# Optimization experiments

Hardware: AMD Instinct MI355X
Metric: run time of the kernel (lower is better)

## Reference

```python
import jax, jax.numpy as jnp
import numpy as np

V = 16000      # vocab_size
D = 256        # embedding_dim
H = 512        # hidden_size (bi-LSTM concat)
HD = H // 2    # per-direction hidden
LAB = 32       # labelset_size (30 tags + START/STOP)
T = 512        # seq length
B = 128        # batch
START = 30
STOP = 31
NEG = -10000.0


def setup_inputs() -> dict:
    key = jax.random.key(0)
    ks = jax.random.split(key, 16)
    sc = 0.05
    emb = jax.random.normal(ks[0], (V, D), jnp.float32) * 0.1
    W_ih_f = jax.random.normal(ks[1], (4 * HD, D), jnp.float32) * sc
    W_hh_f = jax.random.normal(ks[2], (4 * HD, HD), jnp.float32) * sc
    b_f = jax.random.normal(ks[3], (4 * HD,), jnp.float32) * sc  # b_ih + b_hh combined
    W_ih_b = jax.random.normal(ks[4], (4 * HD, D), jnp.float32) * sc
    W_hh_b = jax.random.normal(ks[5], (4 * HD, HD), jnp.float32) * sc
    b_b = jax.random.normal(ks[6], (4 * HD,), jnp.float32) * sc
    Wo = jax.random.normal(ks[7], (LAB, H), jnp.float32) * sc
    bo = jnp.zeros((LAB,), jnp.float32)
    transitions = jax.random.normal(ks[8], (LAB, LAB), jnp.float32)
    transitions = transitions.at[STOP, :].set(NEG).at[:, START].set(NEG)
    h0 = jax.random.normal(ks[9], (2, B, HD), jnp.float32)  # init_hidden() uses randn
    c0 = jax.random.normal(ks[10], (2, B, HD), jnp.float32)
    sentences = jax.random.randint(ks[11], (T, B), 0, V, dtype=jnp.int32)
    labels = jax.random.randint(ks[12], (T, B), 0, 30, dtype=jnp.int32)
    masks = jnp.ones((T, B), dtype=bool)
    return {"emb": emb, "W_ih_f": W_ih_f, "W_hh_f": W_hh_f, "b_f": b_f,
            "W_ih_b": W_ih_b, "W_hh_b": W_hh_b, "b_b": b_b,
            "Wo": Wo, "bo": bo, "transitions": transitions,
            "h0": h0, "c0": c0,
            "sentences": sentences, "labels": labels, "masks": masks}


def _lstm_dir(xproj, h0, c0, W_hh):
    # xproj: [T, B, 4*HD] precomputed input projection (+bias)
    def step(carry, xg):
        h, c = carry
        g = xg + h @ W_hh.T
        i, f, gg, o = jnp.split(g, 4, axis=-1)  # torch gate order i,f,g,o
        i = jax.nn.sigmoid(i); f = jax.nn.sigmoid(f)
        gg = jnp.tanh(gg); o = jax.nn.sigmoid(o)
        c = f * c + i * gg
        h = o * jnp.tanh(c)
        return (h, c), h
    _, hs = jax.lax.scan(step, (h0, c0), xproj)
    return hs  # [T, B, HD]


def reference(emb, W_ih_f, W_hh_f, b_f, W_ih_b, W_hh_b, b_b, Wo, bo,
              transitions, h0, c0, sentences, labels, masks):
    # ---- encoder (dropout omitted: eval-mode determinism) ----
    x = emb[sentences]                                   # [T, B, D]
    xf = jnp.einsum('tbd,gd->tbg', x, W_ih_f) + b_f
    hf = _lstm_dir(xf, h0[0], c0[0], W_hh_f)             # [T, B, HD]
    xb = jnp.einsum('tbd,gd->tbg', x, W_ih_b) + b_b
    hb = _lstm_dir(xb[::-1], h0[1], c0[1], W_hh_b)[::-1]
    out = jnp.concatenate([hf, hb], axis=-1)             # [T, B, H]
    feats = jnp.einsum('tbh,lh->tbl', out, Wo) + bo      # [T, B, LAB]

    # ---- CRF forward algorithm (log partition) ----
    dp0 = jnp.full((B, LAB), NEG, jnp.float32).at[:, START].set(0.0)
    def fstep(dp, inp):
        sc, m = inp  # sc: [B, LAB], m: [B]
        new = jax.scipy.special.logsumexp(
            dp[:, :, None] + transitions[None, :, :] + sc[:, None, :], axis=1)
        return jnp.where(m[:, None], new, dp), None
    dpZ, _ = jax.lax.scan(fstep, dp0, (feats, masks))
    Z = jax.scipy.special.logsumexp(dpZ, axis=1)         # [B]

    # ---- gold path score ----
    lab_ext = jnp.concatenate(
        [jnp.full((1, B), START, labels.dtype), labels], axis=0)  # [T+1, B]
    bidx = jnp.arange(B)
    def gstep(dp, inp):
        sc, m, lp, ln = inp
        tmp = dp + transitions[lp, ln] + sc[bidx, ln]
        return jnp.where(m, tmp, dp), None
    gold, _ = jax.lax.scan(gstep, jnp.zeros((B,), jnp.float32),
                           (feats, masks, lab_ext[:-1], lab_ext[1:]))

    return (Z - gold).sum() / B
```

## Files before the change

kernel.cpp:

```cpp
#include <hip/hip_runtime.h>
#include <stdint.h>

typedef __attribute__((ext_vector_type(8))) short short8;
typedef __attribute__((ext_vector_type(4))) float floatx4;
typedef unsigned int u32;
typedef unsigned short u16;
typedef unsigned long long u64;

#define NROW 65536
#define RING 32

#define OFF_TAGS  64
#define OFF_READY 256
#define OFF_WIH   8192
#define OFF_WHH8  1056768
#define OFF_WO    2105344
#define OFF_RING  2138112
#define OFF_OUT   19177472
#define OFF_FE    86286336
#define WS_NEED   94674944

__device__ __forceinline__ u16 f2bf(float f){
  union { float f; u32 u; } v; v.f = f;
  u32 u = v.u;
  return (u16)((u + 0x7FFFu + ((u >> 16) & 1u)) >> 16);
}
__device__ __forceinline__ float bf2f(u16 h){
  union { u32 u; float f; } v; v.u = ((u32)h) << 16; return v.f;
}
__device__ __forceinline__ u32 pack2(float a, float b){
  return (u32)f2bf(a) | ((u32)f2bf(b) << 16);
}
__device__ __forceinline__ u32 pk_fp8x4(float a, float b, float c, float d){
  u32 lo = __builtin_amdgcn_cvt_pk_fp8_f32(a, b, 0, false);
  return (u32)__builtin_amdgcn_cvt_pk_fp8_f32(c, d, lo, true);
}
__device__ __forceinline__ float sigm(float x){
  return __builtin_amdgcn_rcpf(1.f + __expf(-x));
}
__device__ __forceinline__ float tanh_(float x){
  return 1.f - 2.f * __builtin_amdgcn_rcpf(1.f + __expf(2.f * x));
}
__device__ __forceinline__ floatx4 MF(short8 a, short8 b, floatx4 c){
  return __builtin_amdgcn_mfma_f32_16x16x32_bf16(a, b, c, 0, 0, 0);
}
__device__ __forceinline__ floatx4 MF8(long a, long b, floatx4 c){
  return __builtin_amdgcn_mfma_f32_16x16x32_fp8_fp8(a, b, c, 0, 0, 0);
}
__device__ __forceinline__ void ldsload16(const void* g, void* l){
  __builtin_amdgcn_global_load_lds(
      (const __attribute__((address_space(1))) u32*)g,
      (__attribute__((address_space(3))) u32*)l, 16, 0, 17);
}

__global__ void kdiag(float* out, float v){
  if (threadIdx.x == 0 && blockIdx.x == 0) out[0] = v;
}

__global__ void k0(const float* wf, const float* wb, const float* hf, const float* hb,
                   const float* wo, u16* wih, u16* wob, unsigned char* whh8){
  int e = blockIdx.x * 256 + threadIdx.x;
  if (e < 524288){ wih[e] = f2bf(e < 262144 ? wf[e] : wb[e - 262144]); return; }
  if (e < 540672){ wob[e - 524288] = f2bf(wo[e - 524288]); return; }
  if (e < 1064960){
    int t = e - 540672;
    float w = (t < 262144) ? hf[t] : hb[t - 262144];
    whh8[t] = (unsigned char)(__builtin_amdgcn_cvt_pk_fp8_f32(w, w, 0, false) & 0xFF);
  }
}

__launch_bounds__(512, 1)
__global__ void klstm(const float* emb, const int* sent, const u16* wih,
                      const float* bf_, const float* bb_,
                      const unsigned char* whh8, const float* h0, const float* c0,
                      char* ring, u16* outb, u32* ct, u32* ready){
  __shared__ __align__(16) char SH[98304];
  const int tid = threadIdx.x, n = tid >> 6, l15 = tid & 15, q = (tid >> 4) & 3;
  const int bid = blockIdx.x;

  if (bid >= 32){
    const int p = bid - 32, dir = p & 1;
    const float* bias = dir ? bb_ : bf_;
    int pbud = 1 << 20;
    for (int s = p >> 1; s < 512; s += 112){
      const int t = dir ? 511 - s : s;
      if (s >= 31){
        const int li = tid & 63, need = s - 30;
        bool done = false;
        while (!done && pbud > 0){
          int v = need;
          if (li < 16)
            v = (int)__hip_atomic_load(&ct[dir * 16 + li], __ATOMIC_RELAXED, __HIP_MEMORY_SCOPE_AGENT);
          done = (__ballot(v >= need) == ~0ull);
          if (!done){ __builtin_amdgcn_s_sleep(32); pbud--; }
        }
      }
      {
        int r = tid >> 2, seg = tid & 3;
        const float* er = emb + (size_t)sent[t * 128 + r] * 256 + seg * 64;
        #pragma unroll
        for (int i = 0; i < 8; i++){
          float4 a = *(const float4*)(er + i * 8);
          float4 b = *(const float4*)(er + i * 8 + 4);
          u32 g[4] = { pack2(a.x, a.y), pack2(a.z, a.w), pack2(b.x, b.y), pack2(b.z, b.w) };
          *(uint4*)&SH[((seg * 8 + i) * 128 + r) * 16] = *(uint4*)g;
        }
      }
      __syncthreads();
      short8 Afr[8];
      #pragma unroll
      for (int ks = 0; ks < 8; ks++)
        Afr[ks] = *(const short8*)&SH[((ks * 4 + q) * 128 + n * 16 + l15) * 16];
      char* slot = ring + (size_t)(dir * RING + (s & (RING - 1))) * 262144;
      for (int nt = 0; nt < 16; nt++){
        __syncthreads();
        {
          int h3 = tid >> 6, r = tid & 63;
          const u16* wsrc = wih + (size_t)(dir * 1024 + nt * 64 + r) * 256;
          #pragma unroll
          for (int i = 0; i < 4; i++){
            uint4 v = *(const uint4*)(wsrc + (h3 * 4 + i) * 8);
            *(uint4*)&SH[65536 + ((h3 * 4 + i) * 64 + r) * 16] = v;
          }
        }
        __syncthreads();
        floatx4 acc[4];
        #pragma unroll
        for (int jt = 0; jt < 4; jt++) acc[jt] = floatx4{0.f,0.f,0.f,0.f};
        #pragma unroll
        for (int ks = 0; ks < 8; ks++){
          #pragma unroll
          for (int jt = 0; jt < 4; jt++){
            short8 b = *(const short8*)&SH[65536 + ((ks * 4 + q) * 64 + jt * 16 + l15) * 16];
            acc[jt] = MF(Afr[ks], b, acc[jt]);
          }
        }
        #pragma unroll
        for (int jt = 0; jt < 4; jt++){
          int col = nt * 64 + jt * 16 + l15;
          float bv = bias[col];
          u32 lo = pack2(acc[jt][0] + bv, acc[jt][1] + bv);
          u32 hi = pack2(acc[jt][2] + bv, acc[jt][3] + bv);
          u32 pr[2] = { lo, hi };
          *(uint2*)(slot + col * 256 + (n * 16 + q * 4) * 2) = *(uint2*)pr;
        }
      }
      asm volatile("s_waitcnt vmcnt(0)" ::: "memory");
      __syncthreads();
      if (tid == 0){
        __builtin_amdgcn_fence(__ATOMIC_RELEASE, "agent");
        __hip_atomic_store(&ready[dir * 512 + s], 1u, __ATOMIC_RELAXED, __HIP_MEMORY_SCOPE_AGENT);
      }
    }
    return;
  }

  const int dir = bid >> 4, bc = bid & 15;
  const int q_ = q & 1, hh_t = q >> 1;
  const int i4 = l15 & 3, j4 = l15 >> 2;
  const int hid = n * 32 + hh_t * 16 + l15;
  int cbud = 1 << 22;
  const u32 s01 = i4==0?0x00000400u : i4==1?0x00000105u : i4==2?0x06020000u : 0x03070000u;
  const u32 s23 = i4==0?0x04000000u : i4==1?0x01050000u : i4==2?0x00000602u : 0x00000307u;
  const u32 sfn = (i4 < 2) ? 0x07060100u : 0x03020504u;

  long Wf[8][8];
  #pragma unroll
  for (int g = 0; g < 4; g++)
    #pragma unroll
    for (int hh = 0; hh < 2; hh++){
      int j = g * 256 + n * 32 + hh * 16 + l15;
      const unsigned char* wr = whh8 + (size_t)(dir * 1024 + j) * 256;
      #pragma unroll
      for (int ks = 0; ks < 8; ks++)
        Wf[g * 2 + hh][ks] = *(const long*)(wr + ks * 32 + q * 8);
    }
  float creg[4];
  #pragma unroll
  for (int rg = 0; rg < 4; rg++)
    creg[rg] = c0[((size_t)dir * 128 + bc * 8 + q_ * 4 + rg) * 256 + hid];
  #pragma unroll
  for (int o = 0; o < 8192; o += 8192){ }
  {
    uint4 z = {0,0,0,0};
    *(uint4*)&SH[49152 + tid * 16] = z;
  }
  __syncthreads();
  {
    int b = tid >> 6, hid0 = (tid & 63) * 4;
    const float* hr = h0 + ((size_t)dir * 128 + bc * 8 + b) * 256 + hid0;
    u32 d = pk_fp8x4(hr[0], hr[1], hr[2], hr[3]);
    *(u32*)&SH[49152 + (hid0 >> 3) * 128 + b * 8 + (hid0 & 4)] = d;
  }
  #pragma unroll
  for (int pp = 0; pp < 2; pp++){
    while (__hip_atomic_load(&ready[dir * 512 + pp], __ATOMIC_RELAXED, __HIP_MEMORY_SCOPE_AGENT) == 0u
           && --cbud > 0)
      __builtin_amdgcn_s_sleep(8);
    const char* rp = ring + (size_t)(dir * RING + pp) * 262144 + bc * 16;
    char* xb = SH + pp * 16384;
    #pragma unroll
    for (int it = 0; it < 2; it++){
      int col = it * 512 + tid;
      ldsload16(rp + col * 256, xb + col * 16);
    }
  }
  u32 rdyv = __hip_atomic_load(&ready[dir * 512 + 2], __ATOMIC_RELAXED, __HIP_MEMORY_SCOPE_AGENT);
  asm volatile("s_waitcnt vmcnt(0)" ::: "memory");
  __syncthreads();

  int xcur = 0, xn2 = 2;
  for (int s = 0; s < 512; s++){
    const int t = dir ? 511 - s : s;
    u32 rdyn = 1u;
    if (s + 3 < 512)
      rdyn = __hip_atomic_load(&ready[dir * 512 + s + 3], __ATOMIC_RELAXED, __HIP_MEMORY_SCOPE_AGENT);
    if (s + 2 < 512){
      if (rdyv == 0u){
        while (__hip_atomic_load(&ready[dir * 512 + s + 2], __ATOMIC_RELAXED, __HIP_MEMORY_SCOPE_AGENT) == 0u
               && --cbud > 0)
          __builtin_amdgcn_s_sleep(2);
      }
      const char* rp = ring + (size_t)(dir * RING + ((s + 2) & (RING - 1))) * 262144 + bc * 16;
      char* xb = SH + xn2 * 16384;
      #pragma unroll
      for (int it = 0; it < 2; it++){
        int col = it * 512 + tid;
        ldsload16(rp + col * 256, xb + col * 16);
      }
    }
    rdyv = rdyn;

    const char* hb = SH + 49152 + (s & 1) * 4096;
    long Af[8];
    #pragma unroll
    for (int ks = 0; ks < 8; ks++)
      Af[ks] = *(const long*)(hb + ((ks * 4 + q) * 16 + l15) * 8);
    floatx4 acc[8];
    #pragma unroll
    for (int i = 0; i < 8; i++) acc[i] = floatx4{0.f,0.f,0.f,0.f};
    #pragma unroll
    for (int ks = 0; ks < 8; ks++){
      #pragma unroll
      for (int i = 0; i < 8; i++)
        acc[i] = MF8(Af[ks], Wf[i][ks], acc[i]);
    }

    float v[4][4];
    #pragma unroll
    for (int g = 0; g < 4; g++)
      #pragma unroll
      for (int rg = 0; rg < 4; rg++){
        float hi = __shfl(acc[g * 2 + 1][rg], tid & 31);
        v[g][rg] = (q >= 2) ? hi : acc[g * 2 + 0][rg];
      }

    const char* xb0 = SH + xcur * 16384;
    u64 xg[4];
    #pragma unroll
    for (int g = 0; g < 4; g++)
      xg[g] = *(const u64*)(xb0 + (g * 256 + hid) * 16 + q_ * 8);
    float hv[4];
    #pragma unroll
    for (int rg = 0; rg < 4; rg++){
      float gi = v[0][rg] + bf2f((u16)(xg[0] >> (16 * rg)));
      float gf = v[1][rg] + bf2f((u16)(xg[1] >> (16 * rg)));
      float gg = v[2][rg] + bf2f((u16)(xg[2] >> (16 * rg)));
      float go = v[3][rg] + bf2f((u16)(xg[3] >> (16 * rg)));
      gi = sigm(gi); gf = sigm(gf); gg = tanh_(gg); go = sigm(go);
      float c = gf * creg[rg] + gi * gg;
      creg[rg] = c;
      hv[rg] = go * tanh_(c);
      outb[((size_t)t * 128 + bc * 8 + q_ * 4 + rg) * 512 + dir * 256 + hid] = f2bf(hv[rg]);
    }
    {
      u32 X = pk_fp8x4(hv[0], hv[1], hv[2], hv[3]);
      u32 r1 = __shfl_xor(X, 1), r2 = __shfl_xor(X, 2), r3 = __shfl_xor(X, 3);
      u32 p01 = __builtin_amdgcn_perm(r1, X, s01);
      u32 p23 = __builtin_amdgcn_perm(r3, r2, s23);
      u32 outw = __builtin_amdgcn_perm(p23, p01, sfn);
      char* hn = SH + 49152 + ((s + 1) & 1) * 4096;
      int hidg = hh_t * 16 + j4 * 4;
      *(u32*)&hn[((n * 32 + hidg) >> 3) * 128 + (q_ * 4 + i4) * 8 + (hidg & 4)] = outw;
    }
    if (tid == 0)
      __hip_atomic_store(&ct[dir * 16 + bc], (u32)(s + 1), __ATOMIC_RELAXED, __HIP_MEMORY_SCOPE_AGENT);

    if (s < 509){
      asm volatile("s_waitcnt vmcnt(7) lgkmcnt(0)" ::: "memory");
      __builtin_amdgcn_s_barrier();
    } else if (s < 511){
      asm volatile("s_waitcnt vmcnt(0)" ::: "memory");
      __syncthreads();
    }
    xcur = (xcur == 2) ? 0 : xcur + 1;
    xn2  = (xn2  == 2) ? 0 : xn2  + 1;
  }
}

__launch_bounds__(256, 2)
__global__ void k5(const u16* outb, const u16* wob, const float* bo, float* fe){
  const int tid = threadIdx.x, w = tid >> 6, l15 = tid & 15, q = (tid >> 4) & 3;
  const int rows0 = blockIdx.x * 64;
  short8 WoF[2][16];
  #pragma unroll
  for (int jt = 0; jt < 2; jt++)
    #pragma unroll
    for (int ks = 0; ks < 16; ks++)
      WoF[jt][ks] = *(const short8*)(wob + (size_t)(jt * 16 + l15) * 512 + ks * 32 + q * 8);
  floatx4 a5[2] = { floatx4{0.f,0.f,0.f,0.f}, floatx4{0.f,0.f,0.f,0.f} };
  const u16* ar = outb + (size_t)(rows0 + w * 16 + l15) * 512;
  #pragma unroll
  for (int ks = 0; ks < 16; ks++){
    short8 a = *(const short8*)(ar + ks * 32 + q * 8);
    a5[0] = MF(a, WoF[0][ks], a5[0]);
    a5[1] = MF(a, WoF[1][ks], a5[1]);
  }
  #pragma unroll
  for (int jt = 0; jt < 2; jt++){
    float bv = bo[jt * 16 + l15];
    #pragma unroll
    for (int rg = 0; rg < 4; rg++)
      fe[(size_t)(rows0 + w * 16 + q * 4 + rg) * 32 + jt * 16 + l15] = a5[jt][rg] + bv;
  }
}

__global__ void k6(const float* fe, const int* labels, const float* trans, float* accp){
  __shared__ float TrL[1024];
  __shared__ __align__(16) float dpL[4][32];
  const int tid = threadIdx.x, w = tid >> 6, l = tid & 63, j = l & 31, half = l >> 5;
  const int b = blockIdx.x * 4 + w;
  for (int i = tid; i < 1024; i += 256) TrL[i] = trans[i];
  __syncthreads();
  float Trl[16];
  #pragma unroll
  for (int ii = 0; ii < 16; ii++) Trl[ii] = TrL[(half * 16 + ii) * 32 + j];
  if (half == 0) dpL[w][j] = (j == 30) ? 0.f : -10000.f;

  float gold = 0.f; int lp = 30;
  float sc = fe[(size_t)b * 32 + j];
  int lab = labels[b];
  float ndF = 0.f;
  for (int t = 0; t < 512; t++){
    float scN = 0.f; int labN = 0;
    if (t < 511){
      scN = fe[((size_t)(t + 1) * 128 + b) * 32 + j];
      labN = labels[(t + 1) * 128 + b];
    }
    float dpv[16], tt[16];
    {
      const float4 a = *(const float4*)&dpL[w][half * 16 + 0];
      const float4 b4 = *(const float4*)&dpL[w][half * 16 + 4];
      const float4 c4 = *(const float4*)&dpL[w][half * 16 + 8];
      const float4 d4 = *(const float4*)&dpL[w][half * 16 + 12];
      dpv[0]=a.x; dpv[1]=a.y; dpv[2]=a.z; dpv[3]=a.w;
      dpv[4]=b4.x; dpv[5]=b4.y; dpv[6]=b4.z; dpv[7]=b4.w;
      dpv[8]=c4.x; dpv[9]=c4.y; dpv[10]=c4.z; dpv[11]=c4.w;
      dpv[12]=d4.x; dpv[13]=d4.y; dpv[14]=d4.z; dpv[15]=d4.w;
    }
    float m = -3.0e38f;
    #pragma unroll
    for (int ii = 0; ii < 16; ii++){ tt[ii] = dpv[ii] + Trl[ii]; m = fmaxf(m, tt[ii]); }
    float M = fmaxf(m, __shfl_xor(m, 32));
    float ssum = 0.f;
    #pragma unroll
    for (int ii = 0; ii < 16; ii++) ssum += __expf(tt[ii] - M);
    ssum += __shfl_xor(ssum, 32);
    float nd = sc + M + __logf(ssum);
    float scl = __shfl(sc, lab);
    gold += TrL[lp * 32 + lab] + scl;
    lp = lab;
    if (half == 0) dpL[w][j] = nd;
    ndF = nd;
    sc = scN; lab = labN;
  }
  float M2 = ndF, S2 = 1.f;
  #pragma unroll
  for (int off = 1; off < 64; off <<= 1){
    float Mo = __shfl_xor(M2, off), So = __shfl_xor(S2, off);
    float Mn = fmaxf(M2, Mo);
    S2 = S2 * __expf(M2 - Mn) + So * __expf(Mo - Mn);
    M2 = Mn;
  }
  float Z = M2 + __logf(S2 * 0.5f);
  if (l == 0) atomicAdd(accp, Z - gold);
}

__global__ void k7(const float* accp, float* out){
  if (threadIdx.x == 0 && blockIdx.x == 0) out[0] = accp[0] * (1.f / 128.f);
}

extern "C" void kernel_launch(void* const* d_in, const int* in_sizes, int n_in,
                              void* d_out, int out_size, void* d_ws, size_t ws_size,
                              hipStream_t stream){
  float* outp = (float*)d_out;
  if (ws_size < (size_t)WS_NEED){
    hipLaunchKernelGGL(kdiag, dim3(1), dim3(64), 0, stream, outp, (float)ws_size);
    return;
  }
  const float* emb  = (const float*)d_in[0];
  const float* Wihf = (const float*)d_in[1];
  const float* Whhf = (const float*)d_in[2];
  const float* bf_  = (const float*)d_in[3];
  const float* Wihb = (const float*)d_in[4];
  const float* Whhb = (const float*)d_in[5];
  const float* bb_  = (const float*)d_in[6];
  const float* Wo   = (const float*)d_in[7];
  const float* bo   = (const float*)d_in[8];
  const float* trans= (const float*)d_in[9];
  const float* h0   = (const float*)d_in[10];
  const float* c0   = (const float*)d_in[11];
  const int*   sent = (const int*)d_in[12];
  const int*   labels = (const int*)d_in[13];

  char* ws = (char*)d_ws;
  float* accp = (float*)ws;
  u32* ct    = (u32*)(ws + OFF_TAGS);
  u32* ready = (u32*)(ws + OFF_READY);
  u16* wih   = (u16*)(ws + OFF_WIH);
  unsigned char* whh8 = (unsigned char*)(ws + OFF_WHH8);
  u16* wob   = (u16*)(ws + OFF_WO);
  char* ring = ws + OFF_RING;
  u16* outb  = (u16*)(ws + OFF_OUT);
  float* fe  = (float*)(ws + OFF_FE);

  hipMemsetAsync(d_ws, 0, 8192, stream);
  hipLaunchKernelGGL(k0, dim3(4160), dim3(256), 0, stream,
                     Wihf, Wihb, Whhf, Whhb, Wo, wih, wob, whh8);
  hipLaunchKernelGGL(klstm, dim3(256), dim3(512), 0, stream,
                     emb, sent, wih, bf_, bb_, whh8, h0, c0, ring, outb, ct, ready);
  hipLaunchKernelGGL(k5, dim3(1024), dim3(256), 0, stream, outb, wob, bo, fe);
  hipLaunchKernelGGL(k6, dim3(32), dim3(256), 0, stream, fe, labels, trans, accp);
  hipLaunchKernelGGL(k7, dim3(1), dim3(64), 0, stream, accp, outp);
}
```

Baseline: 1.549 ms.

## Double LSTM block width to 1024 threads and relayout input-projection ring

Grows the persistent LSTM kernel blocks from 512 to 1024 threads. Each recurrent wave now handles one gate-row group, with fewer fp8 weight registers and fewer MFMAs per step. The producer blocks split their work into half-steps across 16 waves. The ring buffer is relaid out per batch chunk so each consumer loads one contiguous 16KB tile with a single load per thread. The aim is to cut the per-step serial recurrence latency by spreading it over more waves, at the cost of extra cross-lane shuffles and possible occupancy or co-residency risk for the persistent spin-waiting blocks.

```diff
diff --git a/kernel.cpp b/kernel.cpp
--- a/kernel.cpp
+++ b/kernel.cpp
@@ -69,23 +69,25 @@
   }
 }
 
-__launch_bounds__(512, 1)
+__launch_bounds__(1024, 4)
 __global__ void klstm(const float* emb, const int* sent, const u16* wih,
                       const float* bf_, const float* bb_,
                       const unsigned char* whh8, const float* h0, const float* c0,
                       char* ring, u16* outb, u32* ct, u32* ready){
   __shared__ __align__(16) char SH[98304];
-  const int tid = threadIdx.x, n = tid >> 6, l15 = tid & 15, q = (tid >> 4) & 3;
+  const int tid = threadIdx.x, w = tid >> 6, l = tid & 63, q = l >> 4, l15 = l & 15;
   const int bid = blockIdx.x;
 
   if (bid >= 32){
     const int p = bid - 32, dir = p & 1;
     const float* bias = dir ? bb_ : bf_;
+    const int m = w & 7, ch = w >> 3;
     int pbud = 1 << 20;
-    for (int s = p >> 1; s < 512; s += 112){
+    for (int u = p; u < 1024; u += 224){
+      const int s = u >> 1;
       const int t = dir ? 511 - s : s;
       if (s >= 31){
-        const int li = tid & 63, need = s - 30;
+        const int li = l, need = s - 30;
         bool done = false;
         while (!done && pbud > 0){
           int v = need;
@@ -96,53 +98,55 @@
         }
       }
       {
-        int r = tid >> 2, seg = tid & 3;
-        const float* er = emb + (size_t)sent[t * 128 + r] * 256 + seg * 64;
+        int r = tid >> 3, g0 = tid & 7;
+        const float* er = emb + (size_t)sent[t * 128 + r] * 256;
         #pragma unroll
-        for (int i = 0; i < 8; i++){
-          float4 a = *(const float4*)(er + i * 8);
-          float4 b = *(const float4*)(er + i * 8 + 4);
-          u32 g[4] = { pack2(a.x, a.y), pack2(a.z, a.w), pack2(b.x, b.y), pack2(b.z, b.w) };
-          *(uint4*)&SH[((seg * 8 + i) * 128 + r) * 16] = *(uint4*)g;
+        for (int j = 0; j < 4; j++){
+          int g8 = g0 + j * 8;
+          float4 a = *(const float4*)(er + g8 * 8);
+          float4 b = *(const float4*)(er + g8 * 8 + 4);
+          u32 gg[4] = { pack2(a.x, a.y), pack2(a.z, a.w), pack2(b.x, b.y), pack2(b.z, b.w) };
+          *(uint4*)&SH[(g8 * 128 + r) * 16] = *(uint4*)gg;
         }
       }
       __syncthreads();
       short8 Afr[8];
       #pragma unroll
       for (int ks = 0; ks < 8; ks++)
-        Afr[ks] = *(const short8*)&SH[((ks * 4 + q) * 128 + n * 16 + l15) * 16];
+        Afr[ks] = *(const short8*)&SH[((ks * 4 + q) * 128 + m * 16 + l15) * 16];
       char* slot = ring + (size_t)(dir * RING + (s & (RING - 1))) * 262144;
+      const int bcw = m * 2 + (q >> 1);
       for (int nt = 0; nt < 16; nt++){
         __syncthreads();
         {
-          int h3 = tid >> 6, r = tid & 63;
+          int r = tid & 63, grp = tid >> 6;
           const u16* wsrc = wih + (size_t)(dir * 1024 + nt * 64 + r) * 256;
           #pragma unroll
-          for (int i = 0; i < 4; i++){
-            uint4 v = *(const uint4*)(wsrc + (h3 * 4 + i) * 8);
-            *(uint4*)&SH[65536 + ((h3 * 4 + i) * 64 + r) * 16] = v;
+          for (int i = 0; i < 2; i++){
+            int kg = grp * 2 + i;
+            uint4 v = *(const uint4*)(wsrc + kg * 8);
+            *(uint4*)&SH[65536 + (kg * 64 + r) * 16] = v;
           }
         }
         __syncthreads();
-        floatx4 acc[4];
-        #pragma unroll
-        for (int jt = 0; jt < 4; jt++) acc[jt] = floatx4{0.f,0.f,0.f,0.f};
+        floatx4 acc[2];
+        acc[0] = floatx4{0.f,0.f,0.f,0.f};
+        acc[1] = floatx4{0.f,0.f,0.f,0.f};
         #pragma unroll
         for (int ks = 0; ks < 8; ks++){
           #pragma unroll
-          for (int jt = 0; jt < 4; jt++){
-            short8 b = *(const short8*)&SH[65536 + ((ks * 4 + q) * 64 + jt * 16 + l15) * 16];
+          for (int jt = 0; jt < 2; jt++){
+            short8 b = *(const short8*)&SH[65536 + ((ks * 4 + q) * 64 + ch * 32 + jt * 16 + l15) * 16];
             acc[jt] = MF(Afr[ks], b, acc[jt]);
           }
         }
         #pragma unroll
-        for (int jt = 0; jt < 4; jt++){
-          int col = nt * 64 + jt * 16 + l15;
+        for (int jt = 0; jt < 2; jt++){
+          int col = nt * 64 + ch * 32 + jt * 16 + l15;
           float bv = bias[col];
-          u32 lo = pack2(acc[jt][0] + bv, acc[jt][1] + bv);
-          u32 hi = pack2(acc[jt][2] + bv, acc[jt][3] + bv);
-          u32 pr[2] = { lo, hi };
-          *(uint2*)(slot + col * 256 + (n * 16 + q * 4) * 2) = *(uint2*)pr;
+          u32 pr[2] = { pack2(acc[jt][0] + bv, acc[jt][1] + bv),
+                        pack2(acc[jt][2] + bv, acc[jt][3] + bv) };
+          *(uint2*)(slot + bcw * 16384 + col * 16 + (q & 1) * 8) = *(uint2*)pr;
         }
       }
       asm volatile("s_waitcnt vmcnt(0)" ::: "memory");
@@ -156,54 +160,45 @@
   }
 
   const int dir = bid >> 4, bc = bid & 15;
-  const int q_ = q & 1, hh_t = q >> 1;
+  const int nn = w >> 1, hw = w & 1;
+  const int H0 = nn * 32 + hw * 16, hid = H0 + l15;
+  const int b0loc = (q & 1) * 4 + (q >> 1) * 2;
   const int i4 = l15 & 3, j4 = l15 >> 2;
-  const int hid = n * 32 + hh_t * 16 + l15;
   int cbud = 1 << 22;
   const u32 s01 = i4==0?0x00000400u : i4==1?0x00000105u : i4==2?0x06020000u : 0x03070000u;
   const u32 s23 = i4==0?0x04000000u : i4==1?0x01050000u : i4==2?0x00000602u : 0x00000307u;
   const u32 sfn = (i4 < 2) ? 0x07060100u : 0x03020504u;
 
-  long Wf[8][8];
-  #pragma unroll
-  for (int g = 0; g < 4; g++)
-    #pragma unroll
-    for (int hh = 0; hh < 2; hh++){
-      int j = g * 256 + n * 32 + hh * 16 + l15;
-      const unsigned char* wr = whh8 + (size_t)(dir * 1024 + j) * 256;
-      #pragma unroll
-      for (int ks = 0; ks < 8; ks++)
-        Wf[g * 2 + hh][ks] = *(const long*)(wr + ks * 32 + q * 8);
-    }
-  float creg[4];
-  #pragma unroll
-  for (int rg = 0; rg < 4; rg++)
-    creg[rg] = c0[((size_t)dir * 128 + bc * 8 + q_ * 4 + rg) * 256 + hid];
-  #pragma unroll
-  for (int o = 0; o < 8192; o += 8192){ }
+  long Wf[4][8];
+  #pragma unroll
+  for (int g = 0; g < 4; g++){
+    const unsigned char* wr = whh8 + (size_t)(dir * 1024 + g * 256 + hid) * 256;
+    #pragma unroll
+    for (int ks = 0; ks < 8; ks++)
+      Wf[g][ks] = *(const long*)(wr + ks * 32 + q * 8);
+  }
+  float creg[2];
+  #pragma unroll
+  for (int e = 0; e < 2; e++)
+    creg[e] = c0[((size_t)dir * 128 + bc * 8 + b0loc + e) * 256 + hid];
   {
-    uint4 z = {0,0,0,0};
-    *(uint4*)&SH[49152 + tid * 16] = z;
-  }
-  __syncthreads();
-  {
-    int b = tid >> 6, hid0 = (tid & 63) * 4;
-    const float* hr = h0 + ((size_t)dir * 128 + bc * 8 + b) * 256 + hid0;
-    u32 d = pk_fp8x4(hr[0], hr[1], hr[2], hr[3]);
-    *(u32*)&SH[49152 + (hid0 >> 3) * 128 + b * 8 + (hid0 & 4)] = d;
+    int a = tid * 4;
+    int kg = a >> 7, rest = a & 127, b = rest >> 3, off4 = a & 4;
+    u32 val0 = 0;
+    if (b < 8){
+      const float* hr = h0 + ((size_t)dir * 128 + bc * 8 + b) * 256 + kg * 8 + off4;
+      val0 = pk_fp8x4(hr[0], hr[1], hr[2], hr[3]);
+    }
+    *(u32*)&SH[49152 + a] = val0;
+    *(u32*)&SH[49152 + 4096 + a] = 0;
   }
   #pragma unroll
   for (int pp = 0; pp < 2; pp++){
     while (__hip_atomic_load(&ready[dir * 512 + pp], __ATOMIC_RELAXED, __HIP_MEMORY_SCOPE_AGENT) == 0u
            && --cbud > 0)
       __builtin_amdgcn_s_sleep(8);
-    const char* rp = ring + (size_t)(dir * RING + pp) * 262144 + bc * 16;
-    char* xb = SH + pp * 16384;
-    #pragma unroll
-    for (int it = 0; it < 2; it++){
-      int col = it * 512 + tid;
-      ldsload16(rp + col * 256, xb + col * 16);
-    }
+    const char* rp = ring + (size_t)(dir * RING + pp) * 262144 + bc * 16384;
+    ldsload16(rp + tid * 16, SH + pp * 16384 + tid * 16);
   }
   u32 rdyv = __hip_atomic_load(&ready[dir * 512 + 2], __ATOMIC_RELAXED, __HIP_MEMORY_SCOPE_AGENT);
   asm volatile("s_waitcnt vmcnt(0)" ::: "memory");
@@ -221,73 +216,71 @@
                && --cbud > 0)
           __builtin_amdgcn_s_sleep(2);
       }
-      const char* rp = ring + (size_t)(dir * RING + ((s + 2) & (RING - 1))) * 262144 + bc * 16;
-      char* xb = SH + xn2 * 16384;
+      const char* rp = ring + (size_t)(dir * RING + ((s + 2) & (RING - 1))) * 262144 + bc * 16384;
+      ldsload16(rp + tid * 16, SH + xn2 * 16384 + tid * 16);
+    }
+    rdyv = rdyn;
+
+    const char* hb = SH + 49152 + (s & 1) * 4096;
+    floatx4 acc[4];
+    #pragma unroll
+    for (int g = 0; g < 4; g++) acc[g] = floatx4{0.f,0.f,0.f,0.f};
+    #pragma unroll
+    for (int ks = 0; ks < 8; ks++){
+      long Af = *(const long*)(hb + ((ks * 4 + q) * 16 + l15) * 8);
       #pragma unroll
-      for (int it = 0; it < 2; it++){
-        int col = it * 512 + tid;
-        ldsload16(rp + col * 256, xb + col * 16);
-      }
-    }
-    rdyv = rdyn;
-
-    const char* hb = SH + 49152 + (s & 1) * 4096;
-    long Af[8];
-    #pragma unroll
-    for (int ks = 0; ks < 8; ks++)
-      Af[ks] = *(const long*)(hb + ((ks * 4 + q) * 16 + l15) * 8);
-    floatx4 acc[8];
-    #pragma unroll
-    for (int i = 0; i < 8; i++) acc[i] = floatx4{0.f,0.f,0.f,0.f};
-    #pragma unroll
-    for (int ks = 0; ks < 8; ks++){
-      #pragma unroll
-      for (int i = 0; i < 8; i++)
-        acc[i] = MF8(Af[ks], Wf[i][ks], acc[i]);
-    }
-
-    float v[4][4];
+      for (int g = 0; g < 4; g++)
+        acc[g] = MF8(Af, Wf[g][ks], acc[g]);
+    }
+
+    float v[4][2];
     #pragma unroll
     for (int g = 0; g < 4; g++)
       #pragma unroll
-      for (int rg = 0; rg < 4; rg++){
-        float hi = __shfl(acc[g * 2 + 1][rg], tid & 31);
-        v[g][rg] = (q >= 2) ? hi : acc[g * 2 + 0][rg];
+      for (int e = 0; e < 2; e++){
+        float hi = __shfl_xor(acc[g][2 + e], 32);
+        v[g][e] = (q >= 2) ? hi : acc[g][e];
       }
 
     const char* xb0 = SH + xcur * 16384;
-    u64 xg[4];
+    u32 xg[4];
     #pragma unroll
     for (int g = 0; g < 4; g++)
-      xg[g] = *(const u64*)(xb0 + (g * 256 + hid) * 16 + q_ * 8);
-    float hv[4];
-    #pragma unroll
-    for (int rg = 0; rg < 4; rg++){
-      float gi = v[0][rg] + bf2f((u16)(xg[0] >> (16 * rg)));
-      float gf = v[1][rg] + bf2f((u16)(xg[1] >> (16 * rg)));
-      float gg = v[2][rg] + bf2f((u16)(xg[2] >> (16 * rg)));
-      float go = v[3][rg] + bf2f((u16)(xg[3] >> (16 * rg)));
+      xg[g] = *(const u32*)(xb0 + ((g * 256 + hid) * 16 + b0loc * 2));
+    float hv[2];
+    #pragma unroll
+    for (int e = 0; e < 2; e++){
+      float gi = v[0][e] + bf2f((u16)(xg[0] >> (16 * e)));
+      float gf = v[1][e] + bf2f((u16)(xg[1] >> (16 * e)));
+      float gg = v[2][e] + bf2f((u16)(xg[2] >> (16 * e)));
+      float go = v[3][e] + bf2f((u16)(xg[3] >> (16 * e)));
       gi = sigm(gi); gf = sigm(gf); gg = tanh_(gg); go = sigm(go);
-      float c = gf * creg[rg] + gi * gg;
-      creg[rg] = c;
-      hv[rg] = go * tanh_(c);
-      outb[((size_t)t * 128 + bc * 8 + q_ * 4 + rg) * 512 + dir * 256 + hid] = f2bf(hv[rg]);
-    }
+      float c = gf * creg[e] + gi * gg;
+      creg[e] = c;
+      hv[e] = go * tanh_(c);
+      outb[((size_t)t * 128 + bc * 8 + b0loc + e) * 512 + dir * 256 + hid] = f2bf(hv[e]);
+    }
+
     {
-      u32 X = pk_fp8x4(hv[0], hv[1], hv[2], hv[3]);
-      u32 r1 = __shfl_xor(X, 1), r2 = __shfl_xor(X, 2), r3 = __shfl_xor(X, 3);
-      u32 p01 = __builtin_amdgcn_perm(r1, X, s01);
+      u32 pk = (u32)__builtin_amdgcn_cvt_pk_fp8_f32(hv[0], hv[1], 0, false);
+      u32 pr = __shfl_xor(pk, 32);
+      u32 quad = (q < 2) ? (pk | (pr << 16)) : (pr | (pk << 16));
+      u32 r1 = __shfl_xor(quad, 1), r2 = __shfl_xor(quad, 2), r3 = __shfl_xor(quad, 3);
+      u32 p01 = __builtin_amdgcn_perm(r1, quad, s01);
       u32 p23 = __builtin_amdgcn_perm(r3, r2, s23);
       u32 outw = __builtin_amdgcn_perm(p23, p01, sfn);
       char* hn = SH + 49152 + ((s + 1) & 1) * 4096;
-      int hidg = hh_t * 16 + j4 * 4;
-      *(u32*)&hn[((n * 32 + hidg) >> 3) * 128 + (q_ * 4 + i4) * 8 + (hidg & 4)] = outw;
+      if (q < 2){
+        int bq = q * 4 + i4;
+        int hidg = H0 + j4 * 4;
+        *(u32*)&hn[(hidg >> 3) * 128 + bq * 8 + (hidg & 4)] = outw;
+      }
     }
     if (tid == 0)
       __hip_atomic_store(&ct[dir * 16 + bc], (u32)(s + 1), __ATOMIC_RELAXED, __HIP_MEMORY_SCOPE_AGENT);
 
     if (s < 509){
-      asm volatile("s_waitcnt vmcnt(7) lgkmcnt(0)" ::: "memory");
+      asm volatile("s_waitcnt vmcnt(4) lgkmcnt(0)" ::: "memory");
       __builtin_amdgcn_s_barrier();
     } else if (s < 511){
       asm volatile("s_waitcnt vmcnt(0)" ::: "memory");
@@ -427,7 +420,7 @@
   hipMemsetAsync(d_ws, 0, 8192, stream);
   hipLaunchKernelGGL(k0, dim3(4160), dim3(256), 0, stream,
                      Wihf, Wihb, Whhf, Whhb, Wo, wih, wob, whh8);
-  hipLaunchKernelGGL(klstm, dim3(256), dim3(512), 0, stream,
+  hipLaunchKernelGGL(klstm, dim3(256), dim3(1024), 0, stream,
                      emb, sent, wih, bf_, bb_, whh8, h0, c0, ring, outb, ct, ready);
   hipLaunchKernelGGL(k5, dim3(1024), dim3(256), 0, stream, outb, wob, bo, fe);
   hipLaunchKernelGGL(k6, dim3(32), dim3(256), 0, stream, fe, labels, trans, accp);
```

Result: faster. 1.384 ms (-10.7%).
